# Optimization experiments

Hardware: AMD Instinct MI355X
Metric: run time of the kernel (lower is better)

The kernel has to match this reference:

```python
import jax, jax.numpy as jnp
import numpy as np

NEG_INF = -1e9  # matches tf mask value -1000000000.0
LEAKY_ALPHA = 0.2  # tf.nn.leaky_relu default


def setup_inputs() -> dict:
    key = jax.random.key(0)
    k1, k2, k3, k4 = jax.random.split(key, 4)
    B, N, F, U = 8, 2048, 128, 128
    X = jax.random.normal(k1, (B, N, F), dtype=jnp.float32)
    A = jax.random.randint(k2, (B, N, N), 0, 2, dtype=jnp.int32)
    W = jax.random.normal(k3, (F, U), dtype=jnp.float32) * 0.1
    a = jax.random.normal(k4, (2 * U, 1), dtype=jnp.float32) * 0.1
    return {"X": X, "A": A, "W": W, "a": a}


def reference(X, A, W, a):
    # H = X @ W : [B, N, U]
    H = jnp.einsum('bnf,fu->bnu', X, W)
    U = H.shape[-1]
    # Additive decomposition of the tile+concat: [H_i || H_j] @ a = H_i@a_src + H_j@a_dst
    a_src = a[:U, 0]   # [U]
    a_dst = a[U:, 0]   # [U]
    s = H @ a_src      # [B, N]
    t = H @ a_dst      # [B, N]
    e = s[:, :, None] + t[:, None, :]            # [B, N, N] pairwise logits
    e = jax.nn.leaky_relu(e, negative_slope=LEAKY_ALPHA)
    mask = jnp.where(A > 0, 0.0, NEG_INF).astype(e.dtype)
    attention = jax.nn.softmax(e + mask, axis=-1)  # [B, N, N]
    H_out = jnp.einsum('bij,bju->biu', attention, H)
    return jax.nn.relu(H_out)
```

## Files before the change

### kernel.cpp

```cpp
#include <hip/hip_runtime.h>
#include <hip/hip_bf16.h>


#define NEG_INF -1.0e9f

typedef __bf16 bf16x8 __attribute__((ext_vector_type(8)));
typedef unsigned short ushort8 __attribute__((ext_vector_type(8)));
typedef float f32x4 __attribute__((ext_vector_type(4)));

__device__ __forceinline__ unsigned short f2b(float x) {
    unsigned u = __builtin_bit_cast(unsigned, x);
    u += 0x7fffu + ((u >> 16) & 1u);
    return (unsigned short)(u >> 16);
}

__device__ __forceinline__ void gload_lds16(const void* g, void* l) {
    __builtin_amdgcn_global_load_lds(
        (const __attribute__((address_space(1))) void*)g,
        (__attribute__((address_space(3))) void*)l, 16, 0, 0);
}

__global__ __launch_bounds__(256) void k_wt(const float* __restrict__ W,
                                            unsigned short* __restrict__ WT) {
    int tid = blockIdx.x * 256 + threadIdx.x;
    int u = tid >> 7, f = tid & 127;
    WT[tid] = f2b(W[f * 128 + u]);
}

__global__ __launch_bounds__(256) void k_h(const float* __restrict__ X,
                                           const unsigned short* __restrict__ WT,
                                           const float* __restrict__ a,
                                           unsigned short* __restrict__ HT,
                                           float* __restrict__ sbuf,
                                           float* __restrict__ tbuf) {
    const int tid  = threadIdx.x;
    const int w    = tid >> 6;
    const int lane = tid & 63;
    const int r    = lane & 15;
    const int cg   = lane >> 4;
    const int row0 = blockIdx.x * 64 + w * 16;
    const int b    = row0 >> 11;
    const int n0   = row0 & 2047;
    const int arow = row0 + r;

    f32x4 acc[8] = {};

#pragma unroll
    for (int k0 = 0; k0 < 128; k0 += 32) {
        const float* xp = X + (size_t)arow * 128 + k0 + cg * 8;
        ushort8 xa;
#pragma unroll
        for (int j = 0; j < 8; j++) xa[j] = f2b(xp[j]);
        bf16x8 av = __builtin_bit_cast(bf16x8, xa);
#pragma unroll
        for (int ut = 0; ut < 8; ut++) {
            ushort8 wb = *(const ushort8*)(WT + (size_t)(ut * 16 + r) * 128 + k0 + cg * 8);
            acc[ut] = __builtin_amdgcn_mfma_f32_16x16x32_bf16(
                av, __builtin_bit_cast(bf16x8, wb), acc[ut], 0, 0, 0);
        }
    }

    float sp[4] = {0.f, 0.f, 0.f, 0.f};
    float tp[4] = {0.f, 0.f, 0.f, 0.f};
#pragma unroll
    for (int ut = 0; ut < 8; ut++) {
        int u = ut * 16 + r;
        float as = a[u];
        float ad = a[128 + u];
#pragma unroll
        for (int reg = 0; reg < 4; reg++) {
            float h = acc[ut][reg];
            int nrow = n0 + cg * 4 + reg;
            HT[((size_t)b * 128 + u) * 2048 + nrow] = f2b(h);
            sp[reg] += h * as;
            tp[reg] += h * ad;
        }
    }
#pragma unroll
    for (int msk = 1; msk < 16; msk <<= 1) {
#pragma unroll
        for (int reg = 0; reg < 4; reg++) {
            sp[reg] += __shfl_xor(sp[reg], msk);
            tp[reg] += __shfl_xor(tp[reg], msk);
        }
    }
    if (r == 0) {
#pragma unroll
        for (int reg = 0; reg < 4; reg++) {
            int row = row0 + cg * 4 + reg;
            sbuf[row] = sp[reg];
            tbuf[row] = tp[reg];
        }
    }
}

__global__ __launch_bounds__(512, 2) void k_attn(const int* __restrict__ A,
                                                 const unsigned short* __restrict__ HT,
                                                 const float* __restrict__ sbuf,
                                                 const float* __restrict__ tbuf,
                                                 float* __restrict__ out) {
    __shared__ char smem[32768];
    __shared__ float dS[4][16];

    const int tid  = threadIdx.x;
    const int w    = tid >> 6;
    const int lane = tid & 63;
    const int r    = lane & 15;
    const int cg   = lane >> 4;
    const int g    = w & 3;
    const int h    = w >> 2;
    const int bid  = blockIdx.x;
    const int b    = bid & 7;
    const int it   = bid >> 3;
    const int i0   = it * 64;
    const int rot  = it & 31;

    const int irow = i0 + g * 16 + r;
    const float s_r   = sbuf[b * 2048 + irow];
    const int* Arow   = A + ((size_t)(b * 2048 + irow)) * 2048 + h * 1024;
    const float* trow = tbuf + b * 2048 + h * 1024;
    const unsigned short* Hb = HT + ((size_t)b * 128) * 2048 + h * 1024;

    const int srow0 = g * 32 + (lane >> 2);
    const int csrc  = (lane & 3) ^ ((lane >> 2) & 3);
    char* const stbase = smem + h * 16384;

    f32x4 acc[8] = {};
    float den = 0.f;

    int4 cA0, cA1; float4 cT0, cT1;
    {
        const int j0 = rot * 32;
        gload_lds16(Hb + (size_t)srow0 * 2048 + j0 + csrc * 8,
                    stbase + (g * 2 + 0) * 1024);
        gload_lds16(Hb + (size_t)(srow0 + 16) * 2048 + j0 + csrc * 8,
                    stbase + (g * 2 + 1) * 1024);
        const int off = j0 + cg * 8;
        cA0 = *(const int4*)(Arow + off);
        cA1 = *(const int4*)(Arow + off + 4);
        cT0 = *(const float4*)(trow + off);
        cT1 = *(const float4*)(trow + off + 4);
    }
    __syncthreads();

    for (int k = 0; k < 32; ++k) {
        const int p = k & 1;
        int4 nA0, nA1; float4 nT0, nT1;
        if (k < 31) {
            const int j0n = ((k + 1 + rot) & 31) * 32;
            char* dst = stbase + (p ^ 1) * 8192;
            gload_lds16(Hb + (size_t)srow0 * 2048 + j0n + csrc * 8,
                        dst + (g * 2 + 0) * 1024);
            gload_lds16(Hb + (size_t)(srow0 + 16) * 2048 + j0n + csrc * 8,
                        dst + (g * 2 + 1) * 1024);
            const int off = j0n + cg * 8;
            nA0 = *(const int4*)(Arow + off);
            nA1 = *(const int4*)(Arow + off + 4);
            nT0 = *(const float4*)(trow + off);
            nT1 = *(const float4*)(trow + off + 4);
        }

        int   ai[8] = {cA0.x, cA0.y, cA0.z, cA0.w, cA1.x, cA1.y, cA1.z, cA1.w};
        float tv[8] = {cT0.x, cT0.y, cT0.z, cT0.w, cT1.x, cT1.y, cT1.z, cT1.w};
        bf16x8 pa;
#pragma unroll
        for (int jj = 0; jj < 8; jj++) {
            float x = s_r + tv[jj];
            float e = fmaxf(x, 0.2f * x);
            e = ai[jj] > 0 ? e : NEG_INF;
            float pp = __expf(e - 16.0f);
            den += pp;
            pa[jj] = (__bf16)pp;
        }

        const char* buf = stbase + p * 8192;
#pragma unroll
        for (int ut = 0; ut < 8; ut++) {
            ushort8 hb = *(const ushort8*)(buf + (ut * 16 + r) * 64 +
                                           ((cg ^ (r & 3)) * 16));
            acc[ut] = __builtin_amdgcn_mfma_f32_16x16x32_bf16(
                pa, __builtin_bit_cast(bf16x8, hb), acc[ut], 0, 0, 0);
        }

        if (k < 31) { cA0 = nA0; cA1 = nA1; cT0 = nT0; cT1 = nT1; }
        __syncthreads();
    }

    den += __shfl_xor(den, 16);
    den += __shfl_xor(den, 32);

    float* accS = (float*)smem;
    if (h == 1) {
        if (cg == 0) dS[g][r] = den;
#pragma unroll
        for (int ut = 0; ut < 8; ut++)
#pragma unroll
            for (int reg = 0; reg < 4; reg++)
                accS[(g * 16 + cg * 4 + reg) * 128 + ut * 16 + r] = acc[ut][reg];
    }
    __syncthreads();
    if (h == 0) {
        float dinv[4];
#pragma unroll
        for (int reg = 0; reg < 4; reg++)
            dinv[reg] = 1.0f / (__shfl(den, cg * 4 + reg) + dS[g][cg * 4 + reg]);
#pragma unroll
        for (int ut = 0; ut < 8; ut++) {
#pragma unroll
            for (int reg = 0; reg < 4; reg++) {
                float num = acc[ut][reg] +
                            accS[(g * 16 + cg * 4 + reg) * 128 + ut * 16 + r];
                float o = fmaxf(num * dinv[reg], 0.f);
                out[((size_t)(b * 2048 + i0 + g * 16 + cg * 4 + reg)) * 128 +
                    ut * 16 + r] = o;
            }
        }
    }
}

extern "C" void kernel_launch(void* const* d_in, const int* in_sizes, int n_in,
                              void* d_out, int out_size, void* d_ws, size_t ws_size,
                              hipStream_t stream) {
    const float* X = (const float*)d_in[0];
    const int*   A = (const int*)d_in[1];
    const float* W = (const float*)d_in[2];
    const float* a = (const float*)d_in[3];
    float* out = (float*)d_out;

    char* ws = (char*)d_ws;
    unsigned short* WT  = (unsigned short*)(ws);
    float*          sb  = (float*)(ws + 32768);
    float*          tb  = (float*)(ws + 32768 + 65536);
    unsigned short* HT  = (unsigned short*)(ws + 32768 + 131072);

    k_wt<<<dim3(64), dim3(256), 0, stream>>>(W, WT);
    k_h<<<dim3(256), dim3(256), 0, stream>>>(X, WT, a, HT, sb, tb);
    k_attn<<<dim3(256), dim3(512), 0, stream>>>(A, HT, sb, tb, out);
}
```

Measured before the change: 62.98 us.

## Split attention blocks into 32 rows with four-way key split-K

The attention kernel now processes 32 query rows per block instead of 64 and splits the key dimension four ways across wave pairs, launching 512 blocks instead of 256. This aims to fill the device's compute units, since 256 blocks leave many of the 256 CUs underused or idle. The per-wave H tile staging load doubles to 4 loads per step, and the final reduction merges three partial accumulators through padded shared memory. Each block uses 64KB of LDS, which may limit concurrent blocks per CU despite the raised launch bound, and H is reloaded from global more times overall.

```diff
diff --git a/kernel.cpp b/kernel.cpp
--- a/kernel.cpp
+++ b/kernel.cpp
@@ -94,36 +94,37 @@
     }
 }
 
-__global__ __launch_bounds__(512, 2) void k_attn(const int* __restrict__ A,
+__global__ __launch_bounds__(512, 4) void k_attn(const int* __restrict__ A,
                                                  const unsigned short* __restrict__ HT,
                                                  const float* __restrict__ sbuf,
                                                  const float* __restrict__ tbuf,
                                                  float* __restrict__ out) {
-    __shared__ char smem[32768];
-    __shared__ float dS[4][16];
+    __shared__ char smem[65536];
+    __shared__ float dSm[4][2][16];
 
     const int tid  = threadIdx.x;
     const int w    = tid >> 6;
     const int lane = tid & 63;
     const int r    = lane & 15;
     const int cg   = lane >> 4;
-    const int g    = w & 3;
-    const int h    = w >> 2;
+    const int g    = w & 1;
+    const int jq   = w >> 1;
     const int bid  = blockIdx.x;
     const int b    = bid & 7;
     const int it   = bid >> 3;
-    const int i0   = it * 64;
-    const int rot  = it & 31;
+    const int i0   = it * 32;
+    const int rot  = it & 15;
 
     const int irow = i0 + g * 16 + r;
     const float s_r   = sbuf[b * 2048 + irow];
-    const int* Arow   = A + ((size_t)(b * 2048 + irow)) * 2048 + h * 1024;
-    const float* trow = tbuf + b * 2048 + h * 1024;
-    const unsigned short* Hb = HT + ((size_t)b * 128) * 2048 + h * 1024;
-
-    const int srow0 = g * 32 + (lane >> 2);
-    const int csrc  = (lane & 3) ^ ((lane >> 2) & 3);
-    char* const stbase = smem + h * 16384;
+    const int* Arow   = A + ((size_t)(b * 2048 + irow)) * 2048 + jq * 512;
+    const float* trow = tbuf + b * 2048 + jq * 512;
+    const unsigned short* Hb = HT + ((size_t)b * 128) * 2048 + jq * 512;
+
+    const int srow = (lane >> 2);
+    const int csrc = (lane & 3) ^ ((lane >> 2) & 3);
+    char* const qbase = smem + jq * 16384;
+    const unsigned short* src0 = Hb + (size_t)(g * 64 + srow) * 2048 + csrc * 8;
 
     f32x4 acc[8] = {};
     float den = 0.f;
@@ -131,10 +132,10 @@
     int4 cA0, cA1; float4 cT0, cT1;
     {
         const int j0 = rot * 32;
-        gload_lds16(Hb + (size_t)srow0 * 2048 + j0 + csrc * 8,
-                    stbase + (g * 2 + 0) * 1024);
-        gload_lds16(Hb + (size_t)(srow0 + 16) * 2048 + j0 + csrc * 8,
-                    stbase + (g * 2 + 1) * 1024);
+#pragma unroll
+        for (int i = 0; i < 4; i++)
+            gload_lds16(src0 + (size_t)i * 16 * 2048 + j0,
+                        qbase + (g * 4 + i) * 1024);
         const int off = j0 + cg * 8;
         cA0 = *(const int4*)(Arow + off);
         cA1 = *(const int4*)(Arow + off + 4);
@@ -143,16 +144,16 @@
     }
     __syncthreads();
 
-    for (int k = 0; k < 32; ++k) {
+    for (int k = 0; k < 16; ++k) {
         const int p = k & 1;
         int4 nA0, nA1; float4 nT0, nT1;
-        if (k < 31) {
-            const int j0n = ((k + 1 + rot) & 31) * 32;
-            char* dst = stbase + (p ^ 1) * 8192;
-            gload_lds16(Hb + (size_t)srow0 * 2048 + j0n + csrc * 8,
-                        dst + (g * 2 + 0) * 1024);
-            gload_lds16(Hb + (size_t)(srow0 + 16) * 2048 + j0n + csrc * 8,
-                        dst + (g * 2 + 1) * 1024);
+        if (k < 15) {
+            const int j0n = ((k + 1 + rot) & 15) * 32;
+            char* dst = qbase + (p ^ 1) * 8192;
+#pragma unroll
+            for (int i = 0; i < 4; i++)
+                gload_lds16(src0 + (size_t)i * 16 * 2048 + j0n,
+                            dst + (g * 4 + i) * 1024);
             const int off = j0n + cg * 8;
             nA0 = *(const int4*)(Arow + off);
             nA1 = *(const int4*)(Arow + off + 4);
@@ -173,7 +174,7 @@
             pa[jj] = (__bf16)pp;
         }
 
-        const char* buf = stbase + p * 8192;
+        const char* buf = qbase + p * 8192;
 #pragma unroll
         for (int ut = 0; ut < 8; ut++) {
             ushort8 hb = *(const ushort8*)(buf + (ut * 16 + r) * 64 +
@@ -182,7 +183,7 @@
                 pa, __builtin_bit_cast(bf16x8, hb), acc[ut], 0, 0, 0);
         }
 
-        if (k < 31) { cA0 = nA0; cA1 = nA1; cT0 = nT0; cT1 = nT1; }
+        if (k < 15) { cA0 = nA0; cA1 = nA1; cT0 = nT0; cT1 = nT1; }
         __syncthreads();
     }
 
@@ -190,28 +191,35 @@
     den += __shfl_xor(den, 32);
 
     float* accS = (float*)smem;
-    if (h == 1) {
-        if (cg == 0) dS[g][r] = den;
+    if (cg == 0) dSm[jq][g][r] = den;
+    if (jq != 0) {
+        const int rowIdx = ((jq - 1) * 2 + g) * 16 + cg * 4;
 #pragma unroll
         for (int ut = 0; ut < 8; ut++)
 #pragma unroll
             for (int reg = 0; reg < 4; reg++)
-                accS[(g * 16 + cg * 4 + reg) * 128 + ut * 16 + r] = acc[ut][reg];
+                accS[(rowIdx + reg) * 132 + ut * 16 + r] = acc[ut][reg];
     }
     __syncthreads();
-    if (h == 0) {
+    if (jq == 0) {
         float dinv[4];
 #pragma unroll
-        for (int reg = 0; reg < 4; reg++)
-            dinv[reg] = 1.0f / (__shfl(den, cg * 4 + reg) + dS[g][cg * 4 + reg]);
+        for (int reg = 0; reg < 4; reg++) {
+            const int row = cg * 4 + reg;
+            dinv[reg] = 1.0f / (dSm[0][g][row] + dSm[1][g][row] +
+                                dSm[2][g][row] + dSm[3][g][row]);
+        }
 #pragma unroll
         for (int ut = 0; ut < 8; ut++) {
 #pragma unroll
             for (int reg = 0; reg < 4; reg++) {
-                float num = acc[ut][reg] +
-                            accS[(g * 16 + cg * 4 + reg) * 128 + ut * 16 + r];
+                const int lrow = cg * 4 + reg;
+                float num = acc[ut][reg]
+                          + accS[((0 * 2 + g) * 16 + lrow) * 132 + ut * 16 + r]
+                          + accS[((1 * 2 + g) * 16 + lrow) * 132 + ut * 16 + r]
+                          + accS[((2 * 2 + g) * 16 + lrow) * 132 + ut * 16 + r];
                 float o = fmaxf(num * dinv[reg], 0.f);
-                out[((size_t)(b * 2048 + i0 + g * 16 + cg * 4 + reg)) * 128 +
+                out[((size_t)(b * 2048 + i0 + g * 16 + lrow)) * 128 +
                     ut * 16 + r] = o;
             }
         }
@@ -235,5 +243,5 @@
 
     k_wt<<<dim3(64), dim3(256), 0, stream>>>(W, WT);
     k_h<<<dim3(256), dim3(256), 0, stream>>>(X, WT, a, HT, sb, tb);
-    k_attn<<<dim3(256), dim3(512), 0, stream>>>(A, HT, sb, tb, out);
-}
+    k_attn<<<dim3(512), dim3(512), 0, stream>>>(A, HT, sb, tb, out);
+}
```

Measured after the change: 61.63 us. 1.02x faster.
